# Performance work log

Measured on AMD Instinct MI355X. Metric: run time of the kernel, lower is better.

The kernel has to match this reference:

```python
import jax, jax.numpy as jnp
import numpy as np
from jax import lax

B, C, H, W = 8, 64, 256, 256
WSIZES = [8, 8]
DRATES = [1, 2]
SHIFT = True
CS = C // len(WSIZES)          # split channels = 32
SCALE = CS ** (-0.5)
EPS = 1e-6


def _ln2d(x, w, b):
    # channel-wise LayerNorm over dim 1 (biased variance), per LayerNormFunction
    mu = x.mean(1, keepdims=True)
    var = ((x - mu) ** 2).mean(1, keepdims=True)
    y = (x - mu) / jnp.sqrt(var + EPS)
    return w[None, :, None, None] * y + b[None, :, None, None]


def _conv1d(x, w, pad, dil):
    # x: [b, ci, L], w: [co, ci, k]
    return lax.conv_general_dilated(x, w, (1,), ((pad, pad),), rhs_dilation=(dil,),
                                    dimension_numbers=('NCH', 'OIH', 'NCH'))


def _eca(x, w1, w2, w3, wc):
    # x: [b,c,h,w] -> channel attention [b,c,1,1]
    y = x.mean((2, 3))[:, None, :]                      # [b,1,c]
    y1 = _conv1d(y, w1, 1, 1)
    y2 = _conv1d(y, w2, 2, 2)
    y3 = _conv1d(y, w3, 4, 4)
    y = _conv1d(jnp.concatenate([y1, y2, y3], axis=1), wc, 1, 1)  # [b,1,c]
    return jax.nn.sigmoid(jnp.transpose(y, (0, 2, 1))[..., None])  # [b,c,1,1]


def _conv1x1(x, w):
    # w: [co, ci]
    return jnp.einsum('bchw,oc->bohw', x, w)


def _win(x, ws):
    # [b,c,H,W] -> [(b nh nw), ws*ws, c]
    b, c, h, w = x.shape
    nh, nw = h // ws, w // ws
    x = x.reshape(b, c, nh, ws, nw, ws).transpose(0, 2, 4, 3, 5, 1)
    return x.reshape(b * nh * nw, ws * ws, c)


def _unwin(x, b, nh, nw, ws):
    c = x.shape[-1]
    x = x.reshape(b, nh, nw, ws, ws, c).transpose(0, 5, 1, 3, 2, 4)
    return x.reshape(b, c, nh * ws, nw * ws)


def setup_inputs() -> dict:
    key = jax.random.key(0)
    ks = jax.random.split(key, 16)
    g = lambda k, shape: jax.random.normal(k, shape, jnp.float32) * 0.02
    return {
        'x0': jax.random.normal(ks[0], (B, C, H, W), jnp.float32),
        'ln_w': jnp.ones((C,), jnp.float32),
        'ln_b': jnp.zeros((C,), jnp.float32),
        'dw_w': g(ks[1], (C, 1, 3, 3)),
        'dw_b': jnp.zeros((C,), jnp.float32),
        'eca_w1': g(ks[2], (1, 1, 3)),
        'eca_w2': g(ks[3], (1, 1, 3)),
        'eca_w3': g(ks[4], (1, 1, 3)),
        'eca_wc': g(ks[5], (1, 3, 3)),
        'wq': g(ks[6], (C, C)),
        'wk': g(ks[7], (C, C)),
        'wv': g(ks[8], (C, C)),
        'down_w': g(ks[9], (CS, 1, 2, 2)),
        'down_b': jnp.zeros((CS,), jnp.float32),
        'sa_w': g(ks[10], (1, C)),
        'sa_b': jnp.zeros((1,), jnp.float32),
        'po_w': g(ks[11], (C, C)),
        'po_b': jnp.zeros((C,), jnp.float32),
    }


def reference(x0, ln_w, ln_b, dw_w, dw_b, eca_w1, eca_w2, eca_w3, eca_wc,
              wq, wk, wv, down_w, down_b, sa_w, sa_b, po_w, po_b):
    b, c, h, w = x0.shape
    x = _ln2d(x0, ln_w, ln_b)
    # depthwise 3x3
    x1 = lax.conv_general_dilated(x, dw_w, (1, 1), ((1, 1), (1, 1)),
                                  feature_group_count=c,
                                  dimension_numbers=('NCHW', 'OIHW', 'NCHW'))
    x1 = x1 + dw_b[None, :, None, None]
    ca = _eca(x1, eca_w1, eca_w2, eca_w3, eca_wc)
    vs = jnp.split(_conv1x1(x, wv) * ca, len(WSIZES), axis=1)
    qs = jnp.split(_conv1x1(x, wq), len(WSIZES), axis=1)
    ks_ = jnp.split(_conv1x1(x, wk), len(WSIZES), axis=1)

    ys = []
    for idx in range(len(WSIZES)):
        ws = WSIZES[idx]
        ds = ws // DRATES[idx]
        q = qs[idx]
        if SHIFT:
            q = jnp.roll(q, (-ws // 2, -ws // 2), (2, 3))
        q = _win(q, ws)
        if DRATES[idx] != 1:
            # depthwise 2x2 stride-2 downsample of k, v
            def down(t):
                t = lax.conv_general_dilated(t, down_w, (2, 2), 'VALID',
                                             feature_group_count=CS,
                                             dimension_numbers=('NCHW', 'OIHW', 'NCHW'))
                return t + down_b[None, :, None, None]
            k = down(ks_[idx])
            v = down(vs[idx])
            if SHIFT:
                k = jnp.roll(k, (-ds // 2, -ds // 2), (2, 3))
                v = jnp.roll(v, (-ds // 2, -ds // 2), (2, 3))
            k = _win(k, ds)
            v = _win(v, ds)
        else:
            k, v = ks_[idx], vs[idx]
            if SHIFT:
                k = jnp.roll(k, (-ws // 2, -ws // 2), (2, 3))
                v = jnp.roll(v, (-ws // 2, -ws // 2), (2, 3))
            k = _win(k, ws)
            v = _win(v, ws)
        atn = jax.nn.softmax(jnp.einsum('nqc,nkc->nqk', q, k) * SCALE, axis=-1)
        y_ = jnp.einsum('nqk,nkc->nqc', atn, v)
        y_ = _unwin(y_, b, h // ws, w // ws, ws)
        if SHIFT:
            y_ = jnp.roll(y_, (ws // 2, ws // 2), (2, 3))
        ys.append(y_)

    y = jnp.concatenate(ys, axis=1)
    x1m = jax.nn.sigmoid(_conv1x1(y, sa_w) + sa_b[None, :, None, None]) * x1
    y = _conv1x1(y + x1m, po_w) + po_b[None, :, None, None]
    return y + x0
```

## Files before the change

kernel.cpp:

```cpp
#include <hip/hip_runtime.h>
#include <hip/hip_bf16.h>

using bf16 = __hip_bfloat16;

constexpr int B = 8, C = 64, H = 256, W = 256;
constexpr int HWs = H * W;
constexpr int NPIX = B * H * W;
constexpr long long NELEM = (long long)B * C * H * W;
constexpr int CS = 32;
constexpr int Hd = 128, Wd = 128;
constexpr int HWd = Hd * Wd;
constexpr int NDOWN = B * CS * HWd;
constexpr float EPS = 1e-6f;
constexpr float SCALE = 0.17677669529663687f;

typedef __attribute__((ext_vector_type(8))) short short8v;
typedef __attribute__((ext_vector_type(8))) unsigned short ushort8v;
typedef __attribute__((ext_vector_type(4))) unsigned short ushort4v;
typedef __attribute__((ext_vector_type(4))) float f32x4;

__device__ __forceinline__ float b2f(bf16 v) { return __bfloat162float(v); }
__device__ __forceinline__ bf16 f2b(float v) { return __float2bfloat16(v); }
__device__ __forceinline__ unsigned short f2bu(float v) {
  bf16 t = __float2bfloat16(v);
  unsigned short u;
  __builtin_memcpy(&u, &t, 2);
  return u;
}
__device__ __forceinline__ float bu2f(unsigned short u) {
  bf16 t;
  __builtin_memcpy(&t, &u, 2);
  return __bfloat162float(t);
}
__device__ __forceinline__ short8v pack2(ushort4v a, ushort4v b) {
  short8v r;
  r[0] = (short)a[0]; r[1] = (short)a[1]; r[2] = (short)a[2]; r[3] = (short)a[3];
  r[4] = (short)b[0]; r[5] = (short)b[1]; r[6] = (short)b[2]; r[7] = (short)b[3];
  return r;
}

__global__ __launch_bounds__(256) void qkv_ln_kernel(
    const float* __restrict__ x0, const float* __restrict__ lnw,
    const float* __restrict__ lnb, const float* __restrict__ wq,
    const float* __restrict__ wk, const float* __restrict__ wv,
    unsigned short* __restrict__ xo, unsigned short* __restrict__ q0,
    unsigned short* __restrict__ q1, unsigned short* __restrict__ k0,
    unsigned short* __restrict__ v0, unsigned short* __restrict__ ksp,
    unsigned short* __restrict__ vsp) {
  __shared__ unsigned short sA[4][2560];
  __shared__ unsigned short sB[4][2560];
  int lane = threadIdx.x & 63, wid = threadIdx.x >> 6;
  int lr = lane & 15, lg = lane >> 4;
  unsigned short* A = &sA[wid][0];
  unsigned short* Bs = &sB[wid][0];
  int seg = blockIdx.x * 4 + wid;
  int p0 = seg * 64;
  int b = p0 >> 16;
  int hw0 = p0 & (HWs - 1);
  int r = hw0 >> 8, col0 = hw0 & 255;
  float lwv[16], lbv[16];
#pragma unroll
  for (int ks = 0; ks < 2; ++ks)
#pragma unroll
    for (int j = 0; j < 8; ++j) {
      int c = ks * 32 + lg * 4 + (j & 3) + 16 * (j >> 2);
      lwv[ks * 8 + j] = lnw[c];
      lbv[ks * 8 + j] = lnb[c];
    }
  short8v bx[4][2];
#pragma unroll
  for (int st = 0; st < 4; ++st) {
    const float* xp = x0 + (size_t)b * C * HWs + hw0 + st * 16 + lr;
    float xv[16];
#pragma unroll
    for (int ks = 0; ks < 2; ++ks)
#pragma unroll
      for (int j = 0; j < 8; ++j) {
        int c = ks * 32 + lg * 4 + (j & 3) + 16 * (j >> 2);
        xv[ks * 8 + j] = xp[(size_t)c * HWs];
      }
    float s = 0.f, s2 = 0.f;
#pragma unroll
    for (int i = 0; i < 16; ++i) { s += xv[i]; s2 += xv[i] * xv[i]; }
    s += __shfl_xor(s, 16, 64); s += __shfl_xor(s, 32, 64);
    s2 += __shfl_xor(s2, 16, 64); s2 += __shfl_xor(s2, 32, 64);
    float mu = s * (1.f / 64);
    float var = s2 * (1.f / 64) - mu * mu;
    float rstd = rsqrtf(var + EPS);
#pragma unroll
    for (int ks = 0; ks < 2; ++ks)
#pragma unroll
      for (int j = 0; j < 8; ++j) {
        float xn = lwv[ks * 8 + j] * ((xv[ks * 8 + j] - mu) * rstd) + lbv[ks * 8 + j];
        bx[st][ks][j] = (short)f2bu(xn);
      }
  }
  int rr = (r - 4) & 255;
  int tokr = (rr & 7) * 8;
  int wrow = b * 1024 + (rr >> 3) * 32;
  auto win_store = [&](const unsigned short* src, unsigned short* dst) {
#pragma unroll
    for (int i = 0; i < 4; ++i) {
      int g = i * 4 + (lane >> 4);
      int tl = (lane >> 2) & 3, ch8 = lane & 3;
      int px = g * 4 + tl;
      int ccw = (col0 + px - 4) & 255;
      size_t wb = (size_t)(wrow + (ccw >> 3)) * 2048 +
                  (size_t)(tokr + (ccw & 7)) * 32 + ch8 * 8;
      ushort8v d = *(const ushort8v*)(src + px * 40 + ch8 * 8);
      *(ushort8v*)(dst + wb) = d;
    }
  };
  auto load_wfrag = [&](const float* wsrc, short8v wf[4][2]) {
#pragma unroll
    for (int mt = 0; mt < 4; ++mt)
#pragma unroll
      for (int ks = 0; ks < 2; ++ks) {
        int rowoff = (mt * 16 + lr) * 64 + ks * 32 + lg * 4;
        short8v t;
#pragma unroll
        for (int j = 0; j < 8; ++j) {
          int kj = (j & 3) + 16 * (j >> 2);
          t[j] = (short)f2bu(wsrc[rowoff + kj]);
        }
        wf[mt][ks] = t;
      }
  };
  f32x4 zero = {0.f, 0.f, 0.f, 0.f};
#pragma unroll
  for (int half = 0; half < 2; ++half) {
#pragma unroll
    for (int st = 0; st < 4; ++st) {
      int px = st * 16 + lr;
#pragma unroll
      for (int j = 0; j < 8; ++j) {
        int c = lg * 4 + (j & 3) + 16 * (j >> 2);
        Bs[c * 80 + px] = (unsigned short)bx[st][half][j];
      }
    }
#pragma unroll
    for (int i = 0; i < 4; ++i) {
      int ch = i * 8 + (lane >> 3), pxg = lane & 7;
      ushort8v d = *(const ushort8v*)(Bs + ch * 80 + pxg * 8);
      *(ushort8v*)(xo + ((size_t)b * 64 + half * 32 + ch) * HWs + hw0 + pxg * 8) = d;
    }
  }
  {
    short8v wf[4][2];
    load_wfrag(wq, wf);
#pragma unroll
    for (int st = 0; st < 4; ++st) {
      f32x4 acc[4];
#pragma unroll
      for (int mt = 0; mt < 4; ++mt) {
        acc[mt] = __builtin_amdgcn_mfma_f32_16x16x32_bf16(wf[mt][0], bx[st][0], zero, 0, 0, 0);
        acc[mt] = __builtin_amdgcn_mfma_f32_16x16x32_bf16(wf[mt][1], bx[st][1], acc[mt], 0, 0, 0);
      }
      int px = st * 16 + lr;
#pragma unroll
      for (int mt = 0; mt < 2; ++mt)
#pragma unroll
        for (int i = 0; i < 4; ++i)
          A[px * 40 + mt * 16 + lg * 4 + i] = f2bu(acc[mt][i]);
#pragma unroll
      for (int mt = 2; mt < 4; ++mt)
#pragma unroll
        for (int i = 0; i < 4; ++i)
          Bs[px * 40 + (mt - 2) * 16 + lg * 4 + i] = f2bu(acc[mt][i]);
    }
    win_store(A, q0);
    win_store(Bs, q1);
  }
  {
    short8v wf[4][2];
    load_wfrag(wk, wf);
#pragma unroll
    for (int st = 0; st < 4; ++st) {
      f32x4 acc[4];
#pragma unroll
      for (int mt = 0; mt < 4; ++mt) {
        acc[mt] = __builtin_amdgcn_mfma_f32_16x16x32_bf16(wf[mt][0], bx[st][0], zero, 0, 0, 0);
        acc[mt] = __builtin_amdgcn_mfma_f32_16x16x32_bf16(wf[mt][1], bx[st][1], acc[mt], 0, 0, 0);
      }
      int px = st * 16 + lr;
#pragma unroll
      for (int mt = 0; mt < 2; ++mt)
#pragma unroll
        for (int i = 0; i < 4; ++i)
          A[px * 40 + mt * 16 + lg * 4 + i] = f2bu(acc[mt][i]);
#pragma unroll
      for (int mt = 2; mt < 4; ++mt)
#pragma unroll
        for (int i = 0; i < 4; ++i)
          Bs[((mt - 2) * 16 + lg * 4 + i) * 80 + px] = f2bu(acc[mt][i]);
    }
    win_store(A, k0);
#pragma unroll
    for (int i = 0; i < 4; ++i) {
      int ch = i * 8 + (lane >> 3), pxg = lane & 7;
      ushort8v d = *(const ushort8v*)(Bs + ch * 80 + pxg * 8);
      *(ushort8v*)(ksp + ((size_t)b * 32 + ch) * HWs + hw0 + pxg * 8) = d;
    }
  }
  {
    short8v wf[4][2];
    load_wfrag(wv, wf);
#pragma unroll
    for (int st = 0; st < 4; ++st) {
      f32x4 acc[4];
#pragma unroll
      for (int mt = 0; mt < 4; ++mt) {
        acc[mt] = __builtin_amdgcn_mfma_f32_16x16x32_bf16(wf[mt][0], bx[st][0], zero, 0, 0, 0);
        acc[mt] = __builtin_amdgcn_mfma_f32_16x16x32_bf16(wf[mt][1], bx[st][1], acc[mt], 0, 0, 0);
      }
      int px = st * 16 + lr;
#pragma unroll
      for (int mt = 0; mt < 2; ++mt)
#pragma unroll
        for (int i = 0; i < 4; ++i)
          A[px * 40 + mt * 16 + lg * 4 + i] = f2bu(acc[mt][i]);
#pragma unroll
      for (int mt = 2; mt < 4; ++mt)
#pragma unroll
        for (int i = 0; i < 4; ++i)
          Bs[((mt - 2) * 16 + lg * 4 + i) * 80 + px] = f2bu(acc[mt][i]);
    }
    win_store(A, v0);
#pragma unroll
    for (int i = 0; i < 4; ++i) {
      int ch = i * 8 + (lane >> 3), pxg = lane & 7;
      ushort8v d = *(const ushort8v*)(Bs + ch * 80 + pxg * 8);
      *(ushort8v*)(vsp + ((size_t)b * 32 + ch) * HWs + hw0 + pxg * 8) = d;
    }
  }
}

__global__ __launch_bounds__(256) void dw_kernel(
    const unsigned short* __restrict__ x, const float* __restrict__ dww,
    const float* __restrict__ dwb, unsigned short* __restrict__ x1,
    float* __restrict__ pool) {
  int tid = threadIdx.x;
  int tx = tid & 15, ty = tid >> 4;
  int h = blockIdx.x * 16 + ty;
  int c = blockIdx.y, b = blockIdx.z;
  const unsigned short* xp = x + ((size_t)b * C + c) * HWs;
  float kk[9];
#pragma unroll
  for (int i = 0; i < 9; ++i) kk[i] = dww[c * 9 + i];
  int w0 = tx * 16;
  float acc[16];
  float bias = dwb[c];
#pragma unroll
  for (int i = 0; i < 16; ++i) acc[i] = bias;
#pragma unroll
  for (int dr = 0; dr < 3; ++dr) {
    int hh = h + dr - 1;
    if (hh < 0 || hh >= H) continue;
    const unsigned short* rp = xp + hh * W;
    ushort8v r0 = *(const ushort8v*)(rp + w0);
    ushort8v r1 = *(const ushort8v*)(rp + w0 + 8);
    float p[18];
    p[0] = (w0 > 0) ? bu2f(rp[w0 - 1]) : 0.f;
    p[17] = (w0 + 16 < W) ? bu2f(rp[w0 + 16]) : 0.f;
#pragma unroll
    for (int i = 0; i < 8; ++i) { p[1 + i] = bu2f(r0[i]); p[9 + i] = bu2f(r1[i]); }
    float k0 = kk[dr * 3], k1 = kk[dr * 3 + 1], k2 = kk[dr * 3 + 2];
#pragma unroll
    for (int i = 0; i < 16; ++i)
      acc[i] += k0 * p[i] + k1 * p[i + 1] + k2 * p[i + 2];
  }
  ushort8v o0, o1;
  float s = 0.f;
#pragma unroll
  for (int i = 0; i < 8; ++i) { o0[i] = f2bu(acc[i]); o1[i] = f2bu(acc[i + 8]); }
#pragma unroll
  for (int i = 0; i < 16; ++i) s += acc[i];
  size_t ob = ((size_t)b * C + c) * HWs + h * W + w0;
  *(ushort8v*)(x1 + ob) = o0;
  *(ushort8v*)(x1 + ob + 8) = o1;
#pragma unroll
  for (int off = 32; off > 0; off >>= 1) s += __shfl_down(s, off, 64);
  __shared__ float red[4];
  if ((tid & 63) == 0) red[tid >> 6] = s;
  __syncthreads();
  if (tid == 0) atomicAdd(&pool[b * C + c], red[0] + red[1] + red[2] + red[3]);
}

__global__ __launch_bounds__(512) void eca_kernel(
    const float* __restrict__ pool, const float* __restrict__ w1,
    const float* __restrict__ w2, const float* __restrict__ w3,
    const float* __restrict__ wc, float* __restrict__ ca) {
  int tid = threadIdx.x;
  int b = tid >> 6, c = tid & 63;
  __shared__ float m[8][64], t1[8][64], t2[8][64], t3[8][64];
  m[b][c] = pool[tid] * (1.f / HWs);
  __syncthreads();
  auto gm = [&](int cc) -> float { return (cc >= 0 && cc < 64) ? m[b][cc] : 0.f; };
  t1[b][c] = w1[0] * gm(c - 1) + w1[1] * gm(c) + w1[2] * gm(c + 1);
  t2[b][c] = w2[0] * gm(c - 2) + w2[1] * gm(c) + w2[2] * gm(c + 2);
  t3[b][c] = w3[0] * gm(c - 4) + w3[1] * gm(c) + w3[2] * gm(c + 4);
  __syncthreads();
  auto g1 = [&](int cc) -> float { return (cc >= 0 && cc < 64) ? t1[b][cc] : 0.f; };
  auto g2 = [&](int cc) -> float { return (cc >= 0 && cc < 64) ? t2[b][cc] : 0.f; };
  auto g3 = [&](int cc) -> float { return (cc >= 0 && cc < 64) ? t3[b][cc] : 0.f; };
  float z = 0.f;
#pragma unroll
  for (int k = 0; k < 3; ++k) {
    z += wc[0 * 3 + k] * g1(c + k - 1);
    z += wc[1 * 3 + k] * g2(c + k - 1);
    z += wc[2 * 3 + k] * g3(c + k - 1);
  }
  ca[tid] = 1.f / (1.f + __expf(-z));
}

__global__ __launch_bounds__(256) void down_kernel(
    const unsigned short* __restrict__ ksp, const unsigned short* __restrict__ vsp,
    const float* __restrict__ dw, const float* __restrict__ db,
    unsigned short* __restrict__ kdw, unsigned short* __restrict__ vdw) {
  int t = blockIdx.x * 256 + threadIdx.x;
  int wxd = t & 31, i = (t >> 5) & 127, c = (t >> 12) & 31, b = t >> 17;
  const unsigned short* kp = ksp + ((size_t)b * 32 + c) * HWs;
  const unsigned short* vp = vsp + ((size_t)b * 32 + c) * HWs;
  float w00 = dw[c * 4], w01 = dw[c * 4 + 1], w10 = dw[c * 4 + 2], w11 = dw[c * 4 + 3];
  float bias = db[c];
  int rowa = (2 * i) * W, rowb = rowa + W;
  int c0a = (8 * wxd + 4) & 255, c0b = (8 * wxd + 8) & 255;
  ushort4v ka0 = *(const ushort4v*)(kp + rowa + c0a);
  ushort4v ka1 = *(const ushort4v*)(kp + rowa + c0b);
  ushort4v kb0 = *(const ushort4v*)(kp + rowb + c0a);
  ushort4v kb1 = *(const ushort4v*)(kp + rowb + c0b);
  ushort4v va0 = *(const ushort4v*)(vp + rowa + c0a);
  ushort4v va1 = *(const ushort4v*)(vp + rowa + c0b);
  ushort4v vb0 = *(const ushort4v*)(vp + rowb + c0a);
  ushort4v vb1 = *(const ushort4v*)(vp + rowb + c0b);
  int rr = (i - 2) & 127;
  size_t winb = ((size_t)(b * 1024 + (rr >> 2) * 32 + wxd)) * 512;
  int tokrow = (rr & 3) * 4;
  ushort4v hk, hv;
#pragma unroll
  for (int tx = 0; tx < 4; ++tx) {
    float k00, k01, k10, k11, v00, v01, v10, v11;
    if (tx < 2) {
      k00 = bu2f(ka0[2 * tx]); k01 = bu2f(ka0[2 * tx + 1]);
      k10 = bu2f(kb0[2 * tx]); k11 = bu2f(kb0[2 * tx + 1]);
      v00 = bu2f(va0[2 * tx]); v01 = bu2f(va0[2 * tx + 1]);
      v10 = bu2f(vb0[2 * tx]); v11 = bu2f(vb0[2 * tx + 1]);
    } else {
      k00 = bu2f(ka1[2 * (tx - 2)]); k01 = bu2f(ka1[2 * (tx - 2) + 1]);
      k10 = bu2f(kb1[2 * (tx - 2)]); k11 = bu2f(kb1[2 * (tx - 2) + 1]);
      v00 = bu2f(va1[2 * (tx - 2)]); v01 = bu2f(va1[2 * (tx - 2) + 1]);
      v10 = bu2f(vb1[2 * (tx - 2)]); v11 = bu2f(vb1[2 * (tx - 2) + 1]);
    }
    hk[tx] = f2bu(w00 * k00 + w01 * k01 + w10 * k10 + w11 * k11 + bias);
    hv[tx] = f2bu(w00 * v00 + w01 * v01 + w10 * v10 + w11 * v11 + bias);
  }
  *(ushort4v*)(vdw + winb + (size_t)c * 16 + tokrow) = hv;
#pragma unroll
  for (int tx = 0; tx < 4; ++tx)
    kdw[winb + (size_t)(tokrow + tx) * 32 + c] = hk[tx];
}

__global__ __launch_bounds__(256) void attn0_kernel(
    const unsigned short* __restrict__ q0, const unsigned short* __restrict__ k0,
    const unsigned short* __restrict__ v0, const float* __restrict__ ca,
    unsigned short* __restrict__ y) {
  __shared__ unsigned short zs[4][32][72];
  int tid = threadIdx.x;
  int lane = tid & 63, wid = tid >> 6;
  int lr = lane & 15, lg = lane >> 4;
  int widx = blockIdx.x * 4 + wid;
  int b = widx >> 10;
  unsigned short* zw = &zs[wid][0][0];
  float cav[8];
#pragma unroll
  for (int mt = 0; mt < 2; ++mt)
#pragma unroll
    for (int r2 = 0; r2 < 4; ++r2)
      cav[mt * 4 + r2] = ca[b * 64 + mt * 16 + lg * 4 + r2];
  {
    const unsigned short* vp = v0 + (size_t)widx * 2048 + (size_t)lane * 32;
#pragma unroll
    for (int j2 = 0; j2 < 4; ++j2) {
      ushort8v vv = *(const ushort8v*)(vp + j2 * 8);
#pragma unroll
      for (int i = 0; i < 8; ++i) zw[(j2 * 8 + i) * 72 + lane] = vv[i];
    }
  }
  const unsigned short* kw = k0 + (size_t)widx * 2048;
  const unsigned short* qw = q0 + (size_t)widx * 2048;
  short8v kf[4], qf[4];
#pragma unroll
  for (int kt = 0; kt < 4; ++kt) {
    ushort4v a = *(const ushort4v*)(kw + (kt * 16 + lr) * 32 + lg * 4);
    ushort4v b2 = *(const ushort4v*)(kw + (kt * 16 + lr) * 32 + lg * 4 + 16);
    kf[kt] = pack2(a, b2);
  }
#pragma unroll
  for (int qt = 0; qt < 4; ++qt) {
    ushort4v a = *(const ushort4v*)(qw + (qt * 16 + lr) * 32 + lg * 4);
    ushort4v b2 = *(const ushort4v*)(qw + (qt * 16 + lr) * 32 + lg * 4 + 16);
    qf[qt] = pack2(a, b2);
  }
  __syncthreads();
  short8v va[2][2];
#pragma unroll
  for (int mt = 0; mt < 2; ++mt)
#pragma unroll
    for (int ck = 0; ck < 2; ++ck) {
      ushort4v a = *(const ushort4v*)&zw[(mt * 16 + lr) * 72 + ck * 32 + lg * 4];
      ushort4v b2 = *(const ushort4v*)&zw[(mt * 16 + lr) * 72 + ck * 32 + lg * 4 + 16];
      va[mt][ck] = pack2(a, b2);
    }
  f32x4 zero = {0.f, 0.f, 0.f, 0.f};
#pragma unroll
  for (int qt = 0; qt < 4; ++qt) {
    f32x4 st[4];
#pragma unroll
    for (int kt = 0; kt < 4; ++kt)
      st[kt] = __builtin_amdgcn_mfma_f32_16x16x32_bf16(kf[kt], qf[qt], zero, 0, 0, 0);
    float mx = -1e30f;
#pragma unroll
    for (int kt = 0; kt < 4; ++kt)
#pragma unroll
      for (int r2 = 0; r2 < 4; ++r2) mx = fmaxf(mx, st[kt][r2]);
    mx = fmaxf(mx, __shfl_xor(mx, 16, 64));
    mx = fmaxf(mx, __shfl_xor(mx, 32, 64));
    float sum = 0.f;
#pragma unroll
    for (int kt = 0; kt < 4; ++kt)
#pragma unroll
      for (int r2 = 0; r2 < 4; ++r2) {
        float e = __expf(SCALE * (st[kt][r2] - mx));
        st[kt][r2] = e;
        sum += e;
      }
    sum += __shfl_xor(sum, 16, 64);
    sum += __shfl_xor(sum, 32, 64);
    float inv = 1.f / sum;
    short8v pb[2];
#pragma unroll
    for (int ck = 0; ck < 2; ++ck)
#pragma unroll
      for (int j = 0; j < 8; ++j)
        pb[ck][j] = (short)f2bu(st[ck * 2 + (j >> 2)][j & 3]);
#pragma unroll
    for (int mt = 0; mt < 2; ++mt) {
      f32x4 yt = __builtin_amdgcn_mfma_f32_16x16x32_bf16(va[mt][0], pb[0], zero, 0, 0, 0);
      yt = __builtin_amdgcn_mfma_f32_16x16x32_bf16(va[mt][1], pb[1], yt, 0, 0, 0);
#pragma unroll
      for (int r2 = 0; r2 < 4; ++r2)
        zw[(mt * 16 + lg * 4 + r2) * 72 + qt * 16 + lr] = f2bu(yt[r2] * inv * cav[mt * 4 + r2]);
    }
  }
  __syncthreads();
  int widx0 = blockIdx.x * 4;
  int b0 = widx0 >> 10, wy0 = (widx0 >> 5) & 31, wxb = widx0 & 31;
#pragma unroll
  for (int pass = 0; pass < 4; ++pass) {
    int sub = tid & 3, pair = tid >> 2;
    int ch = pair & 31;
    int row = pass * 2 + (pair >> 5);
    ushort8v t8 = *(const ushort8v*)&zs[sub][ch][row * 8];
    int r2 = (wy0 * 8 + row + 4) & 255;
    int colb = wxb * 8 + 4 + sub * 8;
    size_t yb = ((size_t)b0 * C + ch) * HWs + (size_t)r2 * W;
    if (colb <= 248) {
      *(ushort8v*)(y + yb + colb) = t8;
    } else {
      ushort4v lo, hi;
#pragma unroll
      for (int i = 0; i < 4; ++i) { lo[i] = t8[i]; hi[i] = t8[4 + i]; }
      *(ushort4v*)(y + yb + 252) = lo;
      *(ushort4v*)(y + yb) = hi;
    }
  }
}

__global__ __launch_bounds__(256) void attn1_kernel(
    const unsigned short* __restrict__ q1, const unsigned short* __restrict__ kdw,
    const unsigned short* __restrict__ vdw, const float* __restrict__ ca,
    unsigned short* __restrict__ y) {
  __shared__ unsigned short zs[4][32][72];
  int tid = threadIdx.x;
  int lane = tid & 63, wid = tid >> 6;
  int lr = lane & 15, lg = lane >> 4;
  int widx = blockIdx.x * 4 + wid;
  int b = widx >> 10;
  unsigned short* zw = &zs[wid][0][0];
  float cav[8];
#pragma unroll
  for (int mt = 0; mt < 2; ++mt)
#pragma unroll
    for (int r2 = 0; r2 < 4; ++r2)
      cav[mt * 4 + r2] = ca[b * 64 + 32 + mt * 16 + lg * 4 + r2];
  short8v kfr;
  {
    ushort4v a = *(const ushort4v*)(kdw + (size_t)widx * 512 + lr * 32 + lg * 4);
    ushort4v b2 = *(const ushort4v*)(kdw + (size_t)widx * 512 + lr * 32 + lg * 4 + 16);
    kfr = pack2(a, b2);
  }
  short8v va[2];
#pragma unroll
  for (int mt = 0; mt < 2; ++mt) {
    ushort4v a = *(const ushort4v*)(vdw + (size_t)widx * 512 + (mt * 16 + lr) * 16 + lg * 4);
    short8v t;
#pragma unroll
    for (int i = 0; i < 4; ++i) { t[i] = (short)a[i]; t[4 + i] = 0; }
    va[mt] = t;
  }
  const unsigned short* qw = q1 + (size_t)widx * 2048;
  short8v qf[4];
#pragma unroll
  for (int qt = 0; qt < 4; ++qt) {
    ushort4v a = *(const ushort4v*)(qw + (qt * 16 + lr) * 32 + lg * 4);
    ushort4v b2 = *(const ushort4v*)(qw + (qt * 16 + lr) * 32 + lg * 4 + 16);
    qf[qt] = pack2(a, b2);
  }
  f32x4 zero = {0.f, 0.f, 0.f, 0.f};
#pragma unroll
  for (int qt = 0; qt < 4; ++qt) {
    f32x4 st = __builtin_amdgcn_mfma_f32_16x16x32_bf16(kfr, qf[qt], zero, 0, 0, 0);
    float mx = fmaxf(fmaxf(st[0], st[1]), fmaxf(st[2], st[3]));
    mx = fmaxf(mx, __shfl_xor(mx, 16, 64));
    mx = fmaxf(mx, __shfl_xor(mx, 32, 64));
    float sum = 0.f;
#pragma unroll
    for (int r2 = 0; r2 < 4; ++r2) {
      float e = __expf(SCALE * (st[r2] - mx));
      st[r2] = e;
      sum += e;
    }
    sum += __shfl_xor(sum, 16, 64);
    sum += __shfl_xor(sum, 32, 64);
    float inv = 1.f / sum;
    short8v pb;
#pragma unroll
    for (int j = 0; j < 4; ++j) { pb[j] = (short)f2bu(st[j]); pb[4 + j] = 0; }
#pragma unroll
    for (int mt = 0; mt < 2; ++mt) {
      f32x4 yt = __builtin_amdgcn_mfma_f32_16x16x32_bf16(va[mt], pb, zero, 0, 0, 0);
#pragma unroll
      for (int r2 = 0; r2 < 4; ++r2)
        zw[(mt * 16 + lg * 4 + r2) * 72 + qt * 16 + lr] = f2bu(yt[r2] * inv * cav[mt * 4 + r2]);
    }
  }
  __syncthreads();
  int widx0 = blockIdx.x * 4;
  int b0 = widx0 >> 10, wy0 = (widx0 >> 5) & 31, wxb = widx0 & 31;
#pragma unroll
  for (int pass = 0; pass < 4; ++pass) {
    int sub = tid & 3, pair = tid >> 2;
    int ch = pair & 31;
    int row = pass * 2 + (pair >> 5);
    ushort8v t8 = *(const ushort8v*)&zs[sub][ch][row * 8];
    int r2 = (wy0 * 8 + row + 4) & 255;
    int colb = wxb * 8 + 4 + sub * 8;
    size_t yb = ((size_t)b0 * C + 32 + ch) * HWs + (size_t)r2 * W;
    if (colb <= 248) {
      *(ushort8v*)(y + yb + colb) = t8;
    } else {
      ushort4v lo, hi;
#pragma unroll
      for (int i = 0; i < 4; ++i) { lo[i] = t8[i]; hi[i] = t8[4 + i]; }
      *(ushort4v*)(y + yb + 252) = lo;
      *(ushort4v*)(y + yb) = hi;
    }
  }
}

__global__ __launch_bounds__(256) void final_mfma_kernel(
    const unsigned short* __restrict__ y, const unsigned short* __restrict__ x1,
    const float* __restrict__ x0, const float* __restrict__ sa_w,
    const float* __restrict__ sa_b, const float* __restrict__ po_w,
    const float* __restrict__ po_b, float* __restrict__ out) {
  __shared__ unsigned short zs[64][72];
  __shared__ float part[4][64];
  __shared__ float sgs[64];
  int tid = threadIdx.x;
  int lane = tid & 63, wid = tid >> 6;
  int lr = lane & 15, lg = lane >> 4;
  short8v ap[4][2];
#pragma unroll
  for (int mt = 0; mt < 4; ++mt)
#pragma unroll
    for (int ks = 0; ks < 2; ++ks) {
      int rowoff = (mt * 16 + lr) * 64 + ks * 32 + lg * 4;
      short8v tt;
#pragma unroll
      for (int j = 0; j < 8; ++j) {
        int kj = (j & 3) + 16 * (j >> 2);
        tt[j] = (short)f2bu(po_w[rowoff + kj]);
      }
      ap[mt][ks] = tt;
    }
  int cc = tid >> 2, qx = (tid & 3) * 16;
  const int NBLK = NPIX / 64;
  for (int blk = blockIdx.x; blk < NBLK; blk += gridDim.x) {
    int p0 = blk * 64;
    int b = p0 >> 16, hw0 = p0 & (HWs - 1);
    size_t rbase = (size_t)b * C * HWs + (size_t)cc * HWs + hw0 + qx;
    ushort8v y0 = *(const ushort8v*)(y + rbase);
    ushort8v y1 = *(const ushort8v*)(y + rbase + 8);
    ushort8v a0 = *(const ushort8v*)(x1 + rbase);
    ushort8v a1 = *(const ushort8v*)(x1 + rbase + 8);
    *(ushort8v*)&zs[cc][qx] = y0;
    *(ushort8v*)&zs[cc][qx + 8] = y1;
    __syncthreads();
    {
      int p = tid & 63, qr = tid >> 6;
      float s = 0.f;
#pragma unroll
      for (int c2 = 0; c2 < 16; ++c2)
        s += sa_w[qr * 16 + c2] * bu2f(zs[qr * 16 + c2][p]);
      part[qr][p] = s;
    }
    __syncthreads();
    if (tid < 64) {
      float sd = part[0][tid] + part[1][tid] + part[2][tid] + part[3][tid] + sa_b[0];
      sgs[tid] = 1.f / (1.f + __expf(-sd));
    }
    __syncthreads();
    {
      ushort8v z0, z1;
#pragma unroll
      for (int i = 0; i < 8; ++i) {
        z0[i] = f2bu(bu2f(y0[i]) + sgs[qx + i] * bu2f(a0[i]));
        z1[i] = f2bu(bu2f(y1[i]) + sgs[qx + 8 + i] * bu2f(a1[i]));
      }
      *(ushort8v*)&zs[cc][qx] = z0;
      *(ushort8v*)&zs[cc][qx + 8] = z1;
    }
    __syncthreads();
    short8v bz[2];
#pragma unroll
    for (int ks = 0; ks < 2; ++ks) {
      short8v tt;
#pragma unroll
      for (int j = 0; j < 8; ++j) {
        int c2 = ks * 32 + lg * 4 + (j & 3) + 16 * (j >> 2);
        tt[j] = (short)zs[c2][wid * 16 + lr];
      }
      bz[ks] = tt;
    }
    f32x4 zero = {0.f, 0.f, 0.f, 0.f};
    f32x4 acc[4];
#pragma unroll
    for (int mt = 0; mt < 4; ++mt) {
      acc[mt] = __builtin_amdgcn_mfma_f32_16x16x32_bf16(ap[mt][0], bz[0], zero, 0, 0, 0);
      acc[mt] = __builtin_amdgcn_mfma_f32_16x16x32_bf16(ap[mt][1], bz[1], acc[mt], 0, 0, 0);
    }
    size_t pbase = (size_t)b * C * HWs + hw0 + wid * 16 + lr;
#pragma unroll
    for (int mt = 0; mt < 4; ++mt)
#pragma unroll
      for (int i = 0; i < 4; ++i) {
        int o = mt * 16 + lg * 4 + i;
        out[pbase + (size_t)o * HWs] = acc[mt][i] + po_b[o] + x0[pbase + (size_t)o * HWs];
      }
    __syncthreads();
  }
}

extern "C" void kernel_launch(void* const* d_in, const int* in_sizes, int n_in,
                              void* d_out, int out_size, void* d_ws, size_t ws_size,
                              hipStream_t stream) {
  const float* x0    = (const float*)d_in[0];
  const float* ln_w  = (const float*)d_in[1];
  const float* ln_b  = (const float*)d_in[2];
  const float* dw_w  = (const float*)d_in[3];
  const float* dw_b  = (const float*)d_in[4];
  const float* ew1   = (const float*)d_in[5];
  const float* ew2   = (const float*)d_in[6];
  const float* ew3   = (const float*)d_in[7];
  const float* ewc   = (const float*)d_in[8];
  const float* wq    = (const float*)d_in[9];
  const float* wk    = (const float*)d_in[10];
  const float* wv    = (const float*)d_in[11];
  const float* dwn_w = (const float*)d_in[12];
  const float* dwn_b = (const float*)d_in[13];
  const float* sa_w  = (const float*)d_in[14];
  const float* sa_b  = (const float*)d_in[15];
  const float* po_w  = (const float*)d_in[16];
  const float* po_b  = (const float*)d_in[17];
  float* out = (float*)d_out;

  char* ws = (char*)d_ws;
  const size_t NB = (size_t)NELEM * sizeof(bf16);
  const size_t NH = NB / 2;
  const size_t NDB = (size_t)NDOWN * sizeof(bf16);
  bf16* xbuf  = (bf16*)(ws);
  bf16* x1buf = (bf16*)(ws + NB);
  unsigned short* q0b  = (unsigned short*)(ws + 2 * NB);
  unsigned short* q1b  = (unsigned short*)(ws + 2 * NB + NH);
  unsigned short* k0b  = (unsigned short*)(ws + 3 * NB);
  unsigned short* v0b  = (unsigned short*)(ws + 3 * NB + NH);
  unsigned short* kspb = (unsigned short*)(ws + 4 * NB);
  unsigned short* vspb = (unsigned short*)(ws + 4 * NB + NH);
  unsigned short* kdwb = (unsigned short*)(ws + 5 * NB);
  unsigned short* vdwb = (unsigned short*)(ws + 5 * NB + NDB);
  float* pool = (float*)(ws + 5 * NB + 2 * NDB);
  float* cabuf = pool + B * C;
  bf16* ybuf = xbuf;

  hipMemsetAsync(pool, 0, B * C * sizeof(float), stream);
  qkv_ln_kernel<<<2048, 256, 0, stream>>>(x0, ln_w, ln_b, wq, wk, wv,
                                          (unsigned short*)xbuf, q0b, q1b, k0b, v0b,
                                          kspb, vspb);
  dw_kernel<<<dim3(16, C, B), 256, 0, stream>>>((const unsigned short*)xbuf, dw_w, dw_b,
                                                (unsigned short*)x1buf, pool);
  eca_kernel<<<1, 512, 0, stream>>>(pool, ew1, ew2, ew3, ewc, cabuf);
  down_kernel<<<4096, 256, 0, stream>>>(kspb, vspb, dwn_w, dwn_b, kdwb, vdwb);
  attn0_kernel<<<2048, 256, 0, stream>>>(q0b, k0b, v0b, cabuf, (unsigned short*)ybuf);
  attn1_kernel<<<2048, 256, 0, stream>>>(q1b, kdwb, vdwb, cabuf, (unsigned short*)ybuf);
  final_mfma_kernel<<<2048, 256, 0, stream>>>((const unsigned short*)ybuf,
                                              (const unsigned short*)x1buf, x0,
                                              sa_w, sa_b, po_w, po_b, out);
}
```

Measured before the change: 343.2 us.

## Fuse both attention branches and final projection into one per-window kernel

Merges attn0, attn1 and the final sigmoid-gate plus 1x1 projection kernel into a single kernel. Each wave keeps its window's 64-channel attention output in shared memory and applies the spatial gate and output projection there. This removes the bf16 y intermediate round trip through global memory and two kernel launches. In exchange it uses more shared memory per block, and the final output writes now follow the shifted window layout, which makes them less coalesced than the previous contiguous pixel order.

```diff
diff --git a/kernel.cpp b/kernel.cpp
--- a/kernel.cpp
+++ b/kernel.cpp
@@ -360,225 +360,194 @@
     kdw[winb + (size_t)(tokrow + tx) * 32 + c] = hk[tx];
 }
 
-__global__ __launch_bounds__(256) void attn0_kernel(
+__global__ __launch_bounds__(256) void attn_final_kernel(
     const unsigned short* __restrict__ q0, const unsigned short* __restrict__ k0,
-    const unsigned short* __restrict__ v0, const float* __restrict__ ca,
-    unsigned short* __restrict__ y) {
-  __shared__ unsigned short zs[4][32][72];
+    const unsigned short* __restrict__ v0, const unsigned short* __restrict__ q1,
+    const unsigned short* __restrict__ kdw, const unsigned short* __restrict__ vdw,
+    const float* __restrict__ ca, const unsigned short* __restrict__ x1,
+    const float* __restrict__ x0, const float* __restrict__ sa_w,
+    const float* __restrict__ sa_b, const float* __restrict__ po_w,
+    const float* __restrict__ po_b, float* __restrict__ out) {
+  __shared__ unsigned short zs[4][64][72];
+  __shared__ float sgs[4][64];
   int tid = threadIdx.x;
   int lane = tid & 63, wid = tid >> 6;
   int lr = lane & 15, lg = lane >> 4;
   int widx = blockIdx.x * 4 + wid;
-  int b = widx >> 10;
+  int b = widx >> 10, wy = (widx >> 5) & 31, wx = widx & 31;
   unsigned short* zw = &zs[wid][0][0];
-  float cav[8];
-#pragma unroll
-  for (int mt = 0; mt < 2; ++mt)
-#pragma unroll
-    for (int r2 = 0; r2 < 4; ++r2)
-      cav[mt * 4 + r2] = ca[b * 64 + mt * 16 + lg * 4 + r2];
+  f32x4 zero = {0.f, 0.f, 0.f, 0.f};
   {
-    const unsigned short* vp = v0 + (size_t)widx * 2048 + (size_t)lane * 32;
-#pragma unroll
-    for (int j2 = 0; j2 < 4; ++j2) {
-      ushort8v vv = *(const ushort8v*)(vp + j2 * 8);
-#pragma unroll
-      for (int i = 0; i < 8; ++i) zw[(j2 * 8 + i) * 72 + lane] = vv[i];
-    }
-  }
-  const unsigned short* kw = k0 + (size_t)widx * 2048;
-  const unsigned short* qw = q0 + (size_t)widx * 2048;
-  short8v kf[4], qf[4];
-#pragma unroll
-  for (int kt = 0; kt < 4; ++kt) {
-    ushort4v a = *(const ushort4v*)(kw + (kt * 16 + lr) * 32 + lg * 4);
-    ushort4v b2 = *(const ushort4v*)(kw + (kt * 16 + lr) * 32 + lg * 4 + 16);
-    kf[kt] = pack2(a, b2);
-  }
-#pragma unroll
-  for (int qt = 0; qt < 4; ++qt) {
-    ushort4v a = *(const ushort4v*)(qw + (qt * 16 + lr) * 32 + lg * 4);
-    ushort4v b2 = *(const ushort4v*)(qw + (qt * 16 + lr) * 32 + lg * 4 + 16);
-    qf[qt] = pack2(a, b2);
-  }
-  __syncthreads();
-  short8v va[2][2];
-#pragma unroll
-  for (int mt = 0; mt < 2; ++mt)
-#pragma unroll
-    for (int ck = 0; ck < 2; ++ck) {
-      ushort4v a = *(const ushort4v*)&zw[(mt * 16 + lr) * 72 + ck * 32 + lg * 4];
-      ushort4v b2 = *(const ushort4v*)&zw[(mt * 16 + lr) * 72 + ck * 32 + lg * 4 + 16];
-      va[mt][ck] = pack2(a, b2);
-    }
-  f32x4 zero = {0.f, 0.f, 0.f, 0.f};
-#pragma unroll
-  for (int qt = 0; qt < 4; ++qt) {
-    f32x4 st[4];
-#pragma unroll
-    for (int kt = 0; kt < 4; ++kt)
-      st[kt] = __builtin_amdgcn_mfma_f32_16x16x32_bf16(kf[kt], qf[qt], zero, 0, 0, 0);
-    float mx = -1e30f;
-#pragma unroll
-    for (int kt = 0; kt < 4; ++kt)
-#pragma unroll
-      for (int r2 = 0; r2 < 4; ++r2) mx = fmaxf(mx, st[kt][r2]);
-    mx = fmaxf(mx, __shfl_xor(mx, 16, 64));
-    mx = fmaxf(mx, __shfl_xor(mx, 32, 64));
-    float sum = 0.f;
-#pragma unroll
-    for (int kt = 0; kt < 4; ++kt)
+    float cav[8];
+#pragma unroll
+    for (int mt = 0; mt < 2; ++mt)
+#pragma unroll
+      for (int r2 = 0; r2 < 4; ++r2)
+        cav[mt * 4 + r2] = ca[b * 64 + mt * 16 + lg * 4 + r2];
+    {
+      const unsigned short* vp = v0 + (size_t)widx * 2048 + (size_t)lane * 32;
+#pragma unroll
+      for (int j2 = 0; j2 < 4; ++j2) {
+        ushort8v vv = *(const ushort8v*)(vp + j2 * 8);
+#pragma unroll
+        for (int i = 0; i < 8; ++i) zw[(j2 * 8 + i) * 72 + lane] = vv[i];
+      }
+    }
+    const unsigned short* kw = k0 + (size_t)widx * 2048;
+    const unsigned short* qw = q0 + (size_t)widx * 2048;
+    short8v kf[4], qf[4];
+#pragma unroll
+    for (int kt = 0; kt < 4; ++kt) {
+      ushort4v a = *(const ushort4v*)(kw + (kt * 16 + lr) * 32 + lg * 4);
+      ushort4v b2 = *(const ushort4v*)(kw + (kt * 16 + lr) * 32 + lg * 4 + 16);
+      kf[kt] = pack2(a, b2);
+    }
+#pragma unroll
+    for (int qt = 0; qt < 4; ++qt) {
+      ushort4v a = *(const ushort4v*)(qw + (qt * 16 + lr) * 32 + lg * 4);
+      ushort4v b2 = *(const ushort4v*)(qw + (qt * 16 + lr) * 32 + lg * 4 + 16);
+      qf[qt] = pack2(a, b2);
+    }
+    short8v va[2][2];
+#pragma unroll
+    for (int mt = 0; mt < 2; ++mt)
+#pragma unroll
+      for (int ck = 0; ck < 2; ++ck) {
+        ushort4v a = *(const ushort4v*)&zw[(mt * 16 + lr) * 72 + ck * 32 + lg * 4];
+        ushort4v b2 = *(const ushort4v*)&zw[(mt * 16 + lr) * 72 + ck * 32 + lg * 4 + 16];
+        va[mt][ck] = pack2(a, b2);
+      }
+#pragma unroll
+    for (int qt = 0; qt < 4; ++qt) {
+      f32x4 st[4];
+#pragma unroll
+      for (int kt = 0; kt < 4; ++kt)
+        st[kt] = __builtin_amdgcn_mfma_f32_16x16x32_bf16(kf[kt], qf[qt], zero, 0, 0, 0);
+      float mx = -1e30f;
+#pragma unroll
+      for (int kt = 0; kt < 4; ++kt)
+#pragma unroll
+        for (int r2 = 0; r2 < 4; ++r2) mx = fmaxf(mx, st[kt][r2]);
+      mx = fmaxf(mx, __shfl_xor(mx, 16, 64));
+      mx = fmaxf(mx, __shfl_xor(mx, 32, 64));
+      float sum = 0.f;
+#pragma unroll
+      for (int kt = 0; kt < 4; ++kt)
+#pragma unroll
+        for (int r2 = 0; r2 < 4; ++r2) {
+          float e = __expf(SCALE * (st[kt][r2] - mx));
+          st[kt][r2] = e;
+          sum += e;
+        }
+      sum += __shfl_xor(sum, 16, 64);
+      sum += __shfl_xor(sum, 32, 64);
+      float inv = 1.f / sum;
+      short8v pb[2];
+#pragma unroll
+      for (int ck = 0; ck < 2; ++ck)
+#pragma unroll
+        for (int j = 0; j < 8; ++j)
+          pb[ck][j] = (short)f2bu(st[ck * 2 + (j >> 2)][j & 3]);
+#pragma unroll
+      for (int mt = 0; mt < 2; ++mt) {
+        f32x4 yt = __builtin_amdgcn_mfma_f32_16x16x32_bf16(va[mt][0], pb[0], zero, 0, 0, 0);
+        yt = __builtin_amdgcn_mfma_f32_16x16x32_bf16(va[mt][1], pb[1], yt, 0, 0, 0);
+#pragma unroll
+        for (int r2 = 0; r2 < 4; ++r2)
+          zw[(mt * 16 + lg * 4 + r2) * 72 + qt * 16 + lr] =
+              f2bu(yt[r2] * inv * cav[mt * 4 + r2]);
+      }
+    }
+  }
+  {
+    float cav[8];
+#pragma unroll
+    for (int mt = 0; mt < 2; ++mt)
+#pragma unroll
+      for (int r2 = 0; r2 < 4; ++r2)
+        cav[mt * 4 + r2] = ca[b * 64 + 32 + mt * 16 + lg * 4 + r2];
+    short8v kfr;
+    {
+      ushort4v a = *(const ushort4v*)(kdw + (size_t)widx * 512 + lr * 32 + lg * 4);
+      ushort4v b2 = *(const ushort4v*)(kdw + (size_t)widx * 512 + lr * 32 + lg * 4 + 16);
+      kfr = pack2(a, b2);
+    }
+    short8v va1[2];
+#pragma unroll
+    for (int mt = 0; mt < 2; ++mt) {
+      ushort4v a = *(const ushort4v*)(vdw + (size_t)widx * 512 + (mt * 16 + lr) * 16 + lg * 4);
+      short8v t;
+#pragma unroll
+      for (int i = 0; i < 4; ++i) { t[i] = (short)a[i]; t[4 + i] = 0; }
+      va1[mt] = t;
+    }
+    const unsigned short* qw = q1 + (size_t)widx * 2048;
+#pragma unroll
+    for (int qt = 0; qt < 4; ++qt) {
+      short8v qf;
+      {
+        ushort4v a = *(const ushort4v*)(qw + (qt * 16 + lr) * 32 + lg * 4);
+        ushort4v b2 = *(const ushort4v*)(qw + (qt * 16 + lr) * 32 + lg * 4 + 16);
+        qf = pack2(a, b2);
+      }
+      f32x4 st = __builtin_amdgcn_mfma_f32_16x16x32_bf16(kfr, qf, zero, 0, 0, 0);
+      float mx = fmaxf(fmaxf(st[0], st[1]), fmaxf(st[2], st[3]));
+      mx = fmaxf(mx, __shfl_xor(mx, 16, 64));
+      mx = fmaxf(mx, __shfl_xor(mx, 32, 64));
+      float sum = 0.f;
 #pragma unroll
       for (int r2 = 0; r2 < 4; ++r2) {
-        float e = __expf(SCALE * (st[kt][r2] - mx));
-        st[kt][r2] = e;
+        float e = __expf(SCALE * (st[r2] - mx));
+        st[r2] = e;
         sum += e;
       }
-    sum += __shfl_xor(sum, 16, 64);
-    sum += __shfl_xor(sum, 32, 64);
-    float inv = 1.f / sum;
-    short8v pb[2];
-#pragma unroll
-    for (int ck = 0; ck < 2; ++ck)
-#pragma unroll
-      for (int j = 0; j < 8; ++j)
-        pb[ck][j] = (short)f2bu(st[ck * 2 + (j >> 2)][j & 3]);
-#pragma unroll
-    for (int mt = 0; mt < 2; ++mt) {
-      f32x4 yt = __builtin_amdgcn_mfma_f32_16x16x32_bf16(va[mt][0], pb[0], zero, 0, 0, 0);
-      yt = __builtin_amdgcn_mfma_f32_16x16x32_bf16(va[mt][1], pb[1], yt, 0, 0, 0);
-#pragma unroll
-      for (int r2 = 0; r2 < 4; ++r2)
-        zw[(mt * 16 + lg * 4 + r2) * 72 + qt * 16 + lr] = f2bu(yt[r2] * inv * cav[mt * 4 + r2]);
-    }
-  }
-  __syncthreads();
-  int widx0 = blockIdx.x * 4;
-  int b0 = widx0 >> 10, wy0 = (widx0 >> 5) & 31, wxb = widx0 & 31;
-#pragma unroll
-  for (int pass = 0; pass < 4; ++pass) {
-    int sub = tid & 3, pair = tid >> 2;
-    int ch = pair & 31;
-    int row = pass * 2 + (pair >> 5);
-    ushort8v t8 = *(const ushort8v*)&zs[sub][ch][row * 8];
-    int r2 = (wy0 * 8 + row + 4) & 255;
-    int colb = wxb * 8 + 4 + sub * 8;
-    size_t yb = ((size_t)b0 * C + ch) * HWs + (size_t)r2 * W;
-    if (colb <= 248) {
-      *(ushort8v*)(y + yb + colb) = t8;
-    } else {
-      ushort4v lo, hi;
-#pragma unroll
-      for (int i = 0; i < 4; ++i) { lo[i] = t8[i]; hi[i] = t8[4 + i]; }
-      *(ushort4v*)(y + yb + 252) = lo;
-      *(ushort4v*)(y + yb) = hi;
-    }
-  }
-}
-
-__global__ __launch_bounds__(256) void attn1_kernel(
-    const unsigned short* __restrict__ q1, const unsigned short* __restrict__ kdw,
-    const unsigned short* __restrict__ vdw, const float* __restrict__ ca,
-    unsigned short* __restrict__ y) {
-  __shared__ unsigned short zs[4][32][72];
-  int tid = threadIdx.x;
-  int lane = tid & 63, wid = tid >> 6;
-  int lr = lane & 15, lg = lane >> 4;
-  int widx = blockIdx.x * 4 + wid;
-  int b = widx >> 10;
-  unsigned short* zw = &zs[wid][0][0];
-  float cav[8];
-#pragma unroll
-  for (int mt = 0; mt < 2; ++mt)
-#pragma unroll
-    for (int r2 = 0; r2 < 4; ++r2)
-      cav[mt * 4 + r2] = ca[b * 64 + 32 + mt * 16 + lg * 4 + r2];
-  short8v kfr;
+      sum += __shfl_xor(sum, 16, 64);
+      sum += __shfl_xor(sum, 32, 64);
+      float inv = 1.f / sum;
+      short8v pb;
+#pragma unroll
+      for (int j = 0; j < 4; ++j) { pb[j] = (short)f2bu(st[j]); pb[4 + j] = 0; }
+#pragma unroll
+      for (int mt = 0; mt < 2; ++mt) {
+        f32x4 yt = __builtin_amdgcn_mfma_f32_16x16x32_bf16(va1[mt], pb, zero, 0, 0, 0);
+#pragma unroll
+        for (int r2 = 0; r2 < 4; ++r2)
+          zw[(32 + mt * 16 + lg * 4 + r2) * 72 + qt * 16 + lr] =
+              f2bu(yt[r2] * inv * cav[mt * 4 + r2]);
+      }
+    }
+  }
   {
-    ushort4v a = *(const ushort4v*)(kdw + (size_t)widx * 512 + lr * 32 + lg * 4);
-    ushort4v b2 = *(const ushort4v*)(kdw + (size_t)widx * 512 + lr * 32 + lg * 4 + 16);
-    kfr = pack2(a, b2);
-  }
-  short8v va[2];
-#pragma unroll
-  for (int mt = 0; mt < 2; ++mt) {
-    ushort4v a = *(const ushort4v*)(vdw + (size_t)widx * 512 + (mt * 16 + lr) * 16 + lg * 4);
-    short8v t;
-#pragma unroll
-    for (int i = 0; i < 4; ++i) { t[i] = (short)a[i]; t[4 + i] = 0; }
-    va[mt] = t;
-  }
-  const unsigned short* qw = q1 + (size_t)widx * 2048;
-  short8v qf[4];
-#pragma unroll
-  for (int qt = 0; qt < 4; ++qt) {
-    ushort4v a = *(const ushort4v*)(qw + (qt * 16 + lr) * 32 + lg * 4);
-    ushort4v b2 = *(const ushort4v*)(qw + (qt * 16 + lr) * 32 + lg * 4 + 16);
-    qf[qt] = pack2(a, b2);
-  }
-  f32x4 zero = {0.f, 0.f, 0.f, 0.f};
-#pragma unroll
-  for (int qt = 0; qt < 4; ++qt) {
-    f32x4 st = __builtin_amdgcn_mfma_f32_16x16x32_bf16(kfr, qf[qt], zero, 0, 0, 0);
-    float mx = fmaxf(fmaxf(st[0], st[1]), fmaxf(st[2], st[3]));
-    mx = fmaxf(mx, __shfl_xor(mx, 16, 64));
-    mx = fmaxf(mx, __shfl_xor(mx, 32, 64));
-    float sum = 0.f;
-#pragma unroll
-    for (int r2 = 0; r2 < 4; ++r2) {
-      float e = __expf(SCALE * (st[r2] - mx));
-      st[r2] = e;
-      sum += e;
-    }
-    sum += __shfl_xor(sum, 16, 64);
-    sum += __shfl_xor(sum, 32, 64);
-    float inv = 1.f / sum;
-    short8v pb;
-#pragma unroll
-    for (int j = 0; j < 4; ++j) { pb[j] = (short)f2bu(st[j]); pb[4 + j] = 0; }
-#pragma unroll
-    for (int mt = 0; mt < 2; ++mt) {
-      f32x4 yt = __builtin_amdgcn_mfma_f32_16x16x32_bf16(va[mt], pb, zero, 0, 0, 0);
-#pragma unroll
-      for (int r2 = 0; r2 < 4; ++r2)
-        zw[(mt * 16 + lg * 4 + r2) * 72 + qt * 16 + lr] = f2bu(yt[r2] * inv * cav[mt * 4 + r2]);
-    }
-  }
-  __syncthreads();
-  int widx0 = blockIdx.x * 4;
-  int b0 = widx0 >> 10, wy0 = (widx0 >> 5) & 31, wxb = widx0 & 31;
-#pragma unroll
-  for (int pass = 0; pass < 4; ++pass) {
-    int sub = tid & 3, pair = tid >> 2;
-    int ch = pair & 31;
-    int row = pass * 2 + (pair >> 5);
-    ushort8v t8 = *(const ushort8v*)&zs[sub][ch][row * 8];
-    int r2 = (wy0 * 8 + row + 4) & 255;
-    int colb = wxb * 8 + 4 + sub * 8;
-    size_t yb = ((size_t)b0 * C + 32 + ch) * HWs + (size_t)r2 * W;
-    if (colb <= 248) {
-      *(ushort8v*)(y + yb + colb) = t8;
-    } else {
-      ushort4v lo, hi;
-#pragma unroll
-      for (int i = 0; i < 4; ++i) { lo[i] = t8[i]; hi[i] = t8[4 + i]; }
-      *(ushort4v*)(y + yb + 252) = lo;
-      *(ushort4v*)(y + yb) = hi;
-    }
-  }
-}
-
-__global__ __launch_bounds__(256) void final_mfma_kernel(
-    const unsigned short* __restrict__ y, const unsigned short* __restrict__ x1,
-    const float* __restrict__ x0, const float* __restrict__ sa_w,
-    const float* __restrict__ sa_b, const float* __restrict__ po_w,
-    const float* __restrict__ po_b, float* __restrict__ out) {
-  __shared__ unsigned short zs[64][72];
-  __shared__ float part[4][64];
-  __shared__ float sgs[64];
-  int tid = threadIdx.x;
-  int lane = tid & 63, wid = tid >> 6;
-  int lr = lane & 15, lg = lane >> 4;
+    float s = sa_b[0];
+#pragma unroll
+    for (int ch = 0; ch < 64; ++ch)
+      s += sa_w[ch] * bu2f(zw[ch * 72 + lane]);
+    sgs[wid][lane] = 1.f / (1.f + __expf(-s));
+  }
+  int c0 = wx * 8 + 4;
+  bool wrap = (wx == 31);
+  {
+    int ch = lane;
+    const unsigned short* x1p = x1 + ((size_t)b * C + ch) * HWs;
+#pragma unroll
+    for (int trow = 0; trow < 8; ++trow) {
+      int rsp = (wy * 8 + trow + 4) & 255;
+      ushort8v xv;
+      if (!wrap) {
+        xv = *(const ushort8v*)(x1p + rsp * W + c0);
+      } else {
+        ushort4v lo = *(const ushort4v*)(x1p + rsp * W + 252);
+        ushort4v hi = *(const ushort4v*)(x1p + rsp * W);
+#pragma unroll
+        for (int i = 0; i < 4; ++i) { xv[i] = lo[i]; xv[4 + i] = hi[i]; }
+      }
+      ushort8v y8 = *(const ushort8v*)&zw[ch * 72 + trow * 8];
+#pragma unroll
+      for (int i = 0; i < 8; ++i)
+        y8[i] = f2bu(bu2f(y8[i]) + sgs[wid][trow * 8 + i] * bu2f(xv[i]));
+      *(ushort8v*)&zw[ch * 72 + trow * 8] = y8;
+    }
+  }
   short8v ap[4][2];
 #pragma unroll
   for (int mt = 0; mt < 4; ++mt)
@@ -593,44 +562,8 @@
       }
       ap[mt][ks] = tt;
     }
-  int cc = tid >> 2, qx = (tid & 3) * 16;
-  const int NBLK = NPIX / 64;
-  for (int blk = blockIdx.x; blk < NBLK; blk += gridDim.x) {
-    int p0 = blk * 64;
-    int b = p0 >> 16, hw0 = p0 & (HWs - 1);
-    size_t rbase = (size_t)b * C * HWs + (size_t)cc * HWs + hw0 + qx;
-    ushort8v y0 = *(const ushort8v*)(y + rbase);
-    ushort8v y1 = *(const ushort8v*)(y + rbase + 8);
-    ushort8v a0 = *(const ushort8v*)(x1 + rbase);
-    ushort8v a1 = *(const ushort8v*)(x1 + rbase + 8);
-    *(ushort8v*)&zs[cc][qx] = y0;
-    *(ushort8v*)&zs[cc][qx + 8] = y1;
-    __syncthreads();
-    {
-      int p = tid & 63, qr = tid >> 6;
-      float s = 0.f;
-#pragma unroll
-      for (int c2 = 0; c2 < 16; ++c2)
-        s += sa_w[qr * 16 + c2] * bu2f(zs[qr * 16 + c2][p]);
-      part[qr][p] = s;
-    }
-    __syncthreads();
-    if (tid < 64) {
-      float sd = part[0][tid] + part[1][tid] + part[2][tid] + part[3][tid] + sa_b[0];
-      sgs[tid] = 1.f / (1.f + __expf(-sd));
-    }
-    __syncthreads();
-    {
-      ushort8v z0, z1;
-#pragma unroll
-      for (int i = 0; i < 8; ++i) {
-        z0[i] = f2bu(bu2f(y0[i]) + sgs[qx + i] * bu2f(a0[i]));
-        z1[i] = f2bu(bu2f(y1[i]) + sgs[qx + 8 + i] * bu2f(a1[i]));
-      }
-      *(ushort8v*)&zs[cc][qx] = z0;
-      *(ushort8v*)&zs[cc][qx + 8] = z1;
-    }
-    __syncthreads();
+#pragma unroll
+  for (int qt = 0; qt < 4; ++qt) {
     short8v bz[2];
 #pragma unroll
     for (int ks = 0; ks < 2; ++ks) {
@@ -638,26 +571,28 @@
 #pragma unroll
       for (int j = 0; j < 8; ++j) {
         int c2 = ks * 32 + lg * 4 + (j & 3) + 16 * (j >> 2);
-        tt[j] = (short)zs[c2][wid * 16 + lr];
+        tt[j] = (short)zw[c2 * 72 + qt * 16 + lr];
       }
       bz[ks] = tt;
     }
-    f32x4 zero = {0.f, 0.f, 0.f, 0.f};
     f32x4 acc[4];
 #pragma unroll
     for (int mt = 0; mt < 4; ++mt) {
       acc[mt] = __builtin_amdgcn_mfma_f32_16x16x32_bf16(ap[mt][0], bz[0], zero, 0, 0, 0);
       acc[mt] = __builtin_amdgcn_mfma_f32_16x16x32_bf16(ap[mt][1], bz[1], acc[mt], 0, 0, 0);
     }
-    size_t pbase = (size_t)b * C * HWs + hw0 + wid * 16 + lr;
+    int rsp = (wy * 8 + qt * 2 + (lr >> 3) + 4) & 255;
+    int csp = c0 + (lr & 7);
+    if (csp > 255) csp -= 256;
+    size_t pbase = (size_t)b * C * HWs + (size_t)rsp * W + csp;
 #pragma unroll
     for (int mt = 0; mt < 4; ++mt)
 #pragma unroll
       for (int i = 0; i < 4; ++i) {
         int o = mt * 16 + lg * 4 + i;
-        out[pbase + (size_t)o * HWs] = acc[mt][i] + po_b[o] + x0[pbase + (size_t)o * HWs];
-      }
-    __syncthreads();
+        size_t idx = pbase + (size_t)o * HWs;
+        out[idx] = acc[mt][i] + po_b[o] + x0[idx];
+      }
   }
 }
 
@@ -700,7 +635,6 @@
   unsigned short* vdwb = (unsigned short*)(ws + 5 * NB + NDB);
   float* pool = (float*)(ws + 5 * NB + 2 * NDB);
   float* cabuf = pool + B * C;
-  bf16* ybuf = xbuf;
 
   hipMemsetAsync(pool, 0, B * C * sizeof(float), stream);
   qkv_ln_kernel<<<2048, 256, 0, stream>>>(x0, ln_w, ln_b, wq, wk, wv,
@@ -710,9 +644,7 @@
                                                 (unsigned short*)x1buf, pool);
   eca_kernel<<<1, 512, 0, stream>>>(pool, ew1, ew2, ew3, ewc, cabuf);
   down_kernel<<<4096, 256, 0, stream>>>(kspb, vspb, dwn_w, dwn_b, kdwb, vdwb);
-  attn0_kernel<<<2048, 256, 0, stream>>>(q0b, k0b, v0b, cabuf, (unsigned short*)ybuf);
-  attn1_kernel<<<2048, 256, 0, stream>>>(q1b, kdwb, vdwb, cabuf, (unsigned short*)ybuf);
-  final_mfma_kernel<<<2048, 256, 0, stream>>>((const unsigned short*)ybuf,
+  attn_final_kernel<<<2048, 256, 0, stream>>>(q0b, k0b, v0b, q1b, kdwb, vdwb, cabuf,
                                               (const unsigned short*)x1buf, x0,
                                               sa_w, sa_b, po_w, po_b, out);
 }
```

Result: slower. 447.8 us (+30.5%).
